# Performance work log

Measured on AMD Instinct MI355X. Metric: run time of the kernel, lower is better.

Reference implementation:

```python
import jax, jax.numpy as jnp
import numpy as np

B = 2_000_000
H = 4  # hidden size


def gru_cell(x, h, w_ih, w_hh, b_ih, b_hh):
    # torch GRUCell math. w_ih: [3H, in], w_hh: [3H, H]
    gi = x @ w_ih.T + b_ih  # [B, 3H]
    gh = h @ w_hh.T + b_hh  # [B, 3H]
    i_r, i_z, i_n = jnp.split(gi, 3, axis=1)
    h_r, h_z, h_n = jnp.split(gh, 3, axis=1)
    r = jax.nn.sigmoid(i_r + h_r)
    z = jax.nn.sigmoid(i_z + h_z)
    n = jnp.tanh(i_n + r * h_n)
    return (1.0 - z) * n + z * h


def setup_inputs() -> dict:
    key = jax.random.key(0)
    ks = jax.random.split(key, 16)
    s = 0.3  # small init scale
    inp = {
        "x": jax.random.normal(ks[0], (B, 18), dtype=jnp.float32),
        # r_up: GRUCell(2, 4)
        "w_ih_up": jax.random.normal(ks[1], (3 * H, 2), dtype=jnp.float32) * s,
        "w_hh_up": jax.random.normal(ks[2], (3 * H, H), dtype=jnp.float32) * s,
        "b_ih_up": jax.random.normal(ks[3], (3 * H,), dtype=jnp.float32) * s,
        "b_hh_up": jax.random.normal(ks[4], (3 * H,), dtype=jnp.float32) * s,
        # fc_obs_1: Linear(8, 4), fc_obs_2: Linear(4, 4)
        "w1": jax.random.normal(ks[5], (4, 8), dtype=jnp.float32) * s,
        "b1": jax.random.normal(ks[6], (4,), dtype=jnp.float32) * s,
        "w2": jax.random.normal(ks[7], (4, 4), dtype=jnp.float32) * s,
        "b2": jax.random.normal(ks[8], (4,), dtype=jnp.float32) * s,
        # r_down: GRUCell(4, 4)
        "w_ih_dn": jax.random.normal(ks[9], (3 * H, H), dtype=jnp.float32) * s,
        "w_hh_dn": jax.random.normal(ks[10], (3 * H, H), dtype=jnp.float32) * s,
        "b_ih_dn": jax.random.normal(ks[11], (3 * H,), dtype=jnp.float32) * s,
        "b_hh_dn": jax.random.normal(ks[12], (3 * H,), dtype=jnp.float32) * s,
        # fc_out: Linear(5, 1)
        "w_out": jax.random.normal(ks[13], (1, 5), dtype=jnp.float32) * s,
        "b_out": jax.random.normal(ks[14], (1,), dtype=jnp.float32) * s,
    }
    return inp


def reference(x, w_ih_up, w_hh_up, b_ih_up, b_hh_up, w1, b1, w2, b2,
              w_ih_dn, w_hh_dn, b_ih_dn, b_hh_dn, w_out, b_out):
    obs = x[:, :4]
    j = x[:, 4:11]    # [B, 7]
    jd = x[:, 11:18]  # [B, 7]
    b = x.shape[0]

    # upward recurrence over joints i = 6..0
    h = jnp.zeros((b, H), dtype=x.dtype)
    h_up = []
    for i in reversed(range(7)):
        xi = jnp.stack([j[:, i], jd[:, i]], axis=1)  # [B, 2]
        h = gru_cell(xi, h, w_ih_up, w_hh_up, b_ih_up, b_hh_up)
        h_up.append(h)

    # observation MLP fusion
    h = jnp.tanh(jnp.concatenate([obs, h], axis=1) @ w1.T + b1)
    h = jnp.tanh(h @ w2.T + b2)

    # downward recurrence i = 0..6 consuming h_up in append order
    acts = []
    for i in range(7):
        h = gru_cell(h_up[i], h, w_ih_dn, w_hh_dn, b_ih_dn, b_hh_dn)
        a = jnp.concatenate([h, j[:, i:i + 1]], axis=1) @ w_out.T + b_out  # [B, 1]
        acts.append(a)
    return jnp.concatenate(acts, axis=1)  # [B, 7]
```

## Files before the change

kernel.cpp:

```cpp
#include <hip/hip_runtime.h>


typedef float v2f __attribute__((ext_vector_type(2)));

__device__ __forceinline__ v2f mk2(float a, float b) { v2f r; r.x = a; r.y = b; return r; }
__device__ __forceinline__ v2f spl(float s) { return mk2(s, s); }
__device__ __forceinline__ v2f fma2(v2f a, v2f b, v2f c) { return __builtin_elementwise_fma(a, b, c); }

__device__ __forceinline__ float fexp2(float x) {
#if __has_builtin(__builtin_amdgcn_exp2f)
    return __builtin_amdgcn_exp2f(x);
#else
    return __expf(0.6931471805599453f * x);
#endif
}
__device__ __forceinline__ float frcp(float x) { return __builtin_amdgcn_rcpf(x); }

#define LOG2E 1.44269504088896f

__device__ __forceinline__ v2f sig2(v2f g) {
    v2f t = g * spl(-LOG2E);
    v2f e = mk2(fexp2(t.x), fexp2(t.y));
    v2f d = e + spl(1.0f);
    return mk2(frcp(d.x), frcp(d.y));
}
__device__ __forceinline__ v2f tanh2(v2f g) {
    v2f t = g * spl(-2.0f * LOG2E);
    v2f e = mk2(fexp2(t.x), fexp2(t.y));
    v2f d = e + spl(1.0f);
    v2f r = mk2(frcp(d.x), frcp(d.y));
    return fma2(r, spl(2.0f), spl(-1.0f));
}

__device__ __forceinline__ v2f dot4(const float* __restrict__ w, int k,
                                    v2f a, v2f b, v2f acc) {
    acc = fma2(spl(a.x), mk2(w[4 * k + 0], w[4 * k + 4]), acc);
    acc = fma2(spl(a.y), mk2(w[4 * k + 1], w[4 * k + 5]), acc);
    acc = fma2(spl(b.x), mk2(w[4 * k + 2], w[4 * k + 6]), acc);
    acc = fma2(spl(b.y), mk2(w[4 * k + 3], w[4 * k + 7]), acc);
    return acc;
}

__global__ void __launch_bounds__(256) trec_kernel(
    const float* __restrict__ x,
    const float* __restrict__ w_ih_up, const float* __restrict__ w_hh_up,
    const float* __restrict__ b_ih_up, const float* __restrict__ b_hh_up,
    const float* __restrict__ w1, const float* __restrict__ b1,
    const float* __restrict__ w2, const float* __restrict__ b2,
    const float* __restrict__ w_ih_dn, const float* __restrict__ w_hh_dn,
    const float* __restrict__ b_ih_dn, const float* __restrict__ b_hh_dn,
    const float* __restrict__ w_out, const float* __restrict__ b_out,
    float* __restrict__ out, int n)
{
    int row = blockIdx.x * blockDim.x + threadIdx.x;
    if (row >= n) return;

    float xv[18];
    {
        const float2* xp = reinterpret_cast<const float2*>(x + (size_t)row * 18u);
        #pragma unroll
        for (int k = 0; k < 9; ++k) {
            float2 v = xp[k];
            xv[2 * k] = v.x;
            xv[2 * k + 1] = v.y;
        }
    }

    v2f bsum_up[4], bsum_dn[4];
    #pragma unroll
    for (int p = 0; p < 4; ++p) {
        bsum_up[p] = mk2(b_ih_up[2 * p], b_ih_up[2 * p + 1]) + mk2(b_hh_up[2 * p], b_hh_up[2 * p + 1]);
        bsum_dn[p] = mk2(b_ih_dn[2 * p], b_ih_dn[2 * p + 1]) + mk2(b_hh_dn[2 * p], b_hh_dn[2 * p + 1]);
    }
    const v2f bihnA_up = mk2(b_ih_up[8], b_ih_up[9]),  bihnB_up = mk2(b_ih_up[10], b_ih_up[11]);
    const v2f bhhnA_up = mk2(b_hh_up[8], b_hh_up[9]),  bhhnB_up = mk2(b_hh_up[10], b_hh_up[11]);
    const v2f bihnA_dn = mk2(b_ih_dn[8], b_ih_dn[9]),  bihnB_dn = mk2(b_ih_dn[10], b_ih_dn[11]);
    const v2f bhhnA_dn = mk2(b_hh_dn[8], b_hh_dn[9]),  bhhnB_dn = mk2(b_hh_dn[10], b_hh_dn[11]);

    v2f hA = spl(0.f), hB = spl(0.f);
    v2f hupA[7], hupB[7];

    #pragma unroll
    for (int s = 0; s < 7; ++s) {
        const int i = 6 - s;
        const v2f X0 = spl(xv[4 + i]);
        const v2f X1 = spl(xv[11 + i]);

        v2f rz[4];
        #pragma unroll
        for (int p = 0; p < 4; ++p) {
            const int k = 2 * p;
            v2f acc = bsum_up[p];
            acc = fma2(X0, mk2(w_ih_up[2 * k], w_ih_up[2 * k + 2]), acc);
            acc = fma2(X1, mk2(w_ih_up[2 * k + 1], w_ih_up[2 * k + 3]), acc);
            acc = dot4(w_hh_up, k, hA, hB, acc);
            rz[p] = acc;
        }
        v2f rA = sig2(rz[0]), rB = sig2(rz[1]);
        v2f zA = sig2(rz[2]), zB = sig2(rz[3]);

        v2f giA = bihnA_up, giB = bihnB_up;
        giA = fma2(X0, mk2(w_ih_up[16], w_ih_up[18]), giA);
        giA = fma2(X1, mk2(w_ih_up[17], w_ih_up[19]), giA);
        giB = fma2(X0, mk2(w_ih_up[20], w_ih_up[22]), giB);
        giB = fma2(X1, mk2(w_ih_up[21], w_ih_up[23]), giB);
        v2f ghA = dot4(w_hh_up, 8,  hA, hB, bhhnA_up);
        v2f ghB = dot4(w_hh_up, 10, hA, hB, bhhnB_up);
        v2f nA = tanh2(fma2(rA, ghA, giA));
        v2f nB = tanh2(fma2(rB, ghB, giB));

        hA = fma2(zA, hA - nA, nA);
        hB = fma2(zB, hB - nB, nB);
        hupA[s] = hA; hupB[s] = hB;
    }

    {
        float in8[8] = { xv[0], xv[1], xv[2], xv[3], hA.x, hA.y, hB.x, hB.y };
        v2f t1A, t1B;
        {
            v2f a0 = mk2(b1[0], b1[1]), a1 = mk2(b1[2], b1[3]);
            #pragma unroll
            for (int d = 0; d < 8; ++d) {
                a0 = fma2(spl(in8[d]), mk2(w1[d], w1[8 + d]), a0);
                a1 = fma2(spl(in8[d]), mk2(w1[16 + d], w1[24 + d]), a1);
            }
            t1A = tanh2(a0); t1B = tanh2(a1);
        }
        v2f a0 = dot4(w2, 0, t1A, t1B, mk2(b2[0], b2[1]));
        v2f a1 = dot4(w2, 2, t1A, t1B, mk2(b2[2], b2[3]));
        hA = tanh2(a0); hB = tanh2(a1);
    }

    const float wo0 = w_out[0], wo1 = w_out[1], wo2 = w_out[2], wo3 = w_out[3], wo4 = w_out[4];
    const float bo = b_out[0];
    float acts[7];
    #pragma unroll
    for (int i = 0; i < 7; ++i) {
        const v2f xiA = hupA[i], xiB = hupB[i];

        v2f rz[4];
        #pragma unroll
        for (int p = 0; p < 4; ++p) {
            const int k = 2 * p;
            v2f acc = bsum_dn[p];
            acc = dot4(w_ih_dn, k, xiA, xiB, acc);
            acc = dot4(w_hh_dn, k, hA, hB, acc);
            rz[p] = acc;
        }
        v2f rA = sig2(rz[0]), rB = sig2(rz[1]);
        v2f zA = sig2(rz[2]), zB = sig2(rz[3]);

        v2f giA = dot4(w_ih_dn, 8,  xiA, xiB, bihnA_dn);
        v2f giB = dot4(w_ih_dn, 10, xiA, xiB, bihnB_dn);
        v2f ghA = dot4(w_hh_dn, 8,  hA, hB, bhhnA_dn);
        v2f ghB = dot4(w_hh_dn, 10, hA, hB, bhhnB_dn);
        v2f nA = tanh2(fma2(rA, ghA, giA));
        v2f nB = tanh2(fma2(rB, ghB, giB));

        hA = fma2(zA, hA - nA, nA);
        hB = fma2(zB, hB - nB, nB);

        v2f t = fma2(hA, mk2(wo0, wo1), mk2(bo, 0.f));
        t = fma2(hB, mk2(wo2, wo3), t);
        acts[i] = fmaf(xv[4 + i], wo4, t.x + t.y);
    }

    float* op = out + (size_t)row * 7u;
    #pragma unroll
    for (int i = 0; i < 7; ++i) op[i] = acts[i];
}

extern "C" void kernel_launch(void* const* d_in, const int* in_sizes, int n_in,
                              void* d_out, int out_size, void* d_ws, size_t ws_size,
                              hipStream_t stream)
{
    const float* x       = (const float*)d_in[0];
    const float* w_ih_up = (const float*)d_in[1];
    const float* w_hh_up = (const float*)d_in[2];
    const float* b_ih_up = (const float*)d_in[3];
    const float* b_hh_up = (const float*)d_in[4];
    const float* w1      = (const float*)d_in[5];
    const float* b1      = (const float*)d_in[6];
    const float* w2      = (const float*)d_in[7];
    const float* b2      = (const float*)d_in[8];
    const float* w_ih_dn = (const float*)d_in[9];
    const float* w_hh_dn = (const float*)d_in[10];
    const float* b_ih_dn = (const float*)d_in[11];
    const float* b_hh_dn = (const float*)d_in[12];
    const float* w_out   = (const float*)d_in[13];
    const float* b_out   = (const float*)d_in[14];
    float* out = (float*)d_out;

    const int n = in_sizes[0] / 18;
    const int block = 256;
    const int grid = (n + block - 1) / block;

    trec_kernel<<<grid, block, 0, stream>>>(
        x, w_ih_up, w_hh_up, b_ih_up, b_hh_up,
        w1, b1, w2, b2,
        w_ih_dn, w_hh_dn, b_ih_dn, b_hh_dn,
        w_out, b_out, out, n);
}
```

Measured before the change: 112.7 us.

## Use packed fp16 dot2 instructions for GRU matvecs with repacked weights

Adds a tiny repack kernel that sums biases and converts all weights to packed fp16 pairs in the workspace. The main kernel then computes every gate and MLP dot product with v_dot2_f32_f16 on fp16-packed hidden states, inputs and weights, accumulating in fp32. This roughly halves the ALU instruction count and the scalar weight loads, at the cost of fp16 rounding of weights and activations, which may push results past the tolerance, plus one extra launch per call.

```diff
diff --git a/kernel.cpp b/kernel.cpp
--- a/kernel.cpp
+++ b/kernel.cpp
@@ -2,6 +2,7 @@
 
 
 typedef float v2f __attribute__((ext_vector_type(2)));
+typedef __fp16 h2 __attribute__((ext_vector_type(2)));
 
 __device__ __forceinline__ v2f mk2(float a, float b) { v2f r; r.x = a; r.y = b; return r; }
 __device__ __forceinline__ v2f spl(float s) { return mk2(s, s); }
@@ -32,17 +33,19 @@
     return fma2(r, spl(2.0f), spl(-1.0f));
 }
 
-__device__ __forceinline__ v2f dot4(const float* __restrict__ w, int k,
-                                    v2f a, v2f b, v2f acc) {
-    acc = fma2(spl(a.x), mk2(w[4 * k + 0], w[4 * k + 4]), acc);
-    acc = fma2(spl(a.y), mk2(w[4 * k + 1], w[4 * k + 5]), acc);
-    acc = fma2(spl(b.x), mk2(w[4 * k + 2], w[4 * k + 6]), acc);
-    acc = fma2(spl(b.y), mk2(w[4 * k + 3], w[4 * k + 7]), acc);
-    return acc;
-}
-
-__global__ void __launch_bounds__(256) trec_kernel(
-    const float* __restrict__ x,
+__device__ __forceinline__ float fdot2(h2 a, h2 b, float c) {
+#if __has_builtin(__builtin_amdgcn_fdot2)
+    return __builtin_amdgcn_fdot2(a, b, c, false);
+#else
+    return fmaf((float)a.x, (float)b.x, fmaf((float)a.y, (float)b.y, c));
+#endif
+}
+__device__ __forceinline__ h2 pkh(float a, float b) {
+    return __builtin_amdgcn_cvt_pkrtz(a, b);
+}
+
+
+__global__ void repack_kernel(
     const float* __restrict__ w_ih_up, const float* __restrict__ w_hh_up,
     const float* __restrict__ b_ih_up, const float* __restrict__ b_hh_up,
     const float* __restrict__ w1, const float* __restrict__ b1,
@@ -50,10 +53,51 @@
     const float* __restrict__ w_ih_dn, const float* __restrict__ w_hh_dn,
     const float* __restrict__ b_ih_dn, const float* __restrict__ b_hh_dn,
     const float* __restrict__ w_out, const float* __restrict__ b_out,
+    float* __restrict__ ws)
+{
+    const int t = threadIdx.x;
+    if (t < 42) {
+        float v;
+        if      (t < 8)  v = b_ih_up[t] + b_hh_up[t];
+        else if (t < 16) v = b_ih_dn[t - 8] + b_hh_dn[t - 8];
+        else if (t < 20) v = b_ih_up[8 + t - 16];
+        else if (t < 24) v = b_hh_up[8 + t - 20];
+        else if (t < 28) v = b_ih_dn[8 + t - 24];
+        else if (t < 32) v = b_hh_dn[8 + t - 28];
+        else if (t < 36) v = b1[t - 32];
+        else if (t < 40) v = b2[t - 36];
+        else if (t == 40) v = w_out[4];
+        else              v = b_out[0];
+        ws[t] = v;
+    } else if (t < 152) {
+        const int u = t - 42;
+        float a, b;
+        if (u < 12)       { a = w_ih_up[2*u];                          b = w_ih_up[2*u + 1]; }
+        else if (u < 36)  { int v = u - 12, k = v >> 1, e = v & 1;     a = w_hh_up[4*k + 2*e]; b = w_hh_up[4*k + 2*e + 1]; }
+        else if (u < 60)  { int v = u - 36, k = v >> 1, e = v & 1;     a = w_ih_dn[4*k + 2*e]; b = w_ih_dn[4*k + 2*e + 1]; }
+        else if (u < 84)  { int v = u - 60, k = v >> 1, e = v & 1;     a = w_hh_dn[4*k + 2*e]; b = w_hh_dn[4*k + 2*e + 1]; }
+        else if (u < 100) { int v = u - 84, k = v >> 2, c = v & 3;     a = w1[8*k + 2*c];      b = w1[8*k + 2*c + 1]; }
+        else if (u < 108) { int v = u - 100, k = v >> 1, c = v & 1;    a = w2[4*k + 2*c];      b = w2[4*k + 2*c + 1]; }
+        else              { int c = u - 108;                           a = w_out[2*c];         b = w_out[2*c + 1]; }
+        reinterpret_cast<h2*>(ws)[t] = pkh(a, b);
+    }
+}
+
+__global__ void __launch_bounds__(256) trec_kernel(
+    const float* __restrict__ x, const float* __restrict__ sb,
     float* __restrict__ out, int n)
 {
-    int row = blockIdx.x * blockDim.x + threadIdx.x;
+    const int row = blockIdx.x * blockDim.x + threadIdx.x;
     if (row >= n) return;
+
+    const h2* __restrict__ wh = reinterpret_cast<const h2*>(sb + 42);
+    #define WIU(k)    wh[(k)]
+    #define WHU(k,e)  wh[12 + 2*(k) + (e)]
+    #define WID(k,e)  wh[36 + 2*(k) + (e)]
+    #define WHD(k,e)  wh[60 + 2*(k) + (e)]
+    #define W1H(k,c)  wh[84 + 4*(k) + (c)]
+    #define W2H(k,c)  wh[100 + 2*(k) + (c)]
+    #define WOH(c)    wh[108 + (c)]
 
     float xv[18];
     {
@@ -65,109 +109,99 @@
             xv[2 * k + 1] = v.y;
         }
     }
-
-    v2f bsum_up[4], bsum_dn[4];
-    #pragma unroll
-    for (int p = 0; p < 4; ++p) {
-        bsum_up[p] = mk2(b_ih_up[2 * p], b_ih_up[2 * p + 1]) + mk2(b_hh_up[2 * p], b_hh_up[2 * p + 1]);
-        bsum_dn[p] = mk2(b_ih_dn[2 * p], b_ih_dn[2 * p + 1]) + mk2(b_hh_dn[2 * p], b_hh_dn[2 * p + 1]);
-    }
-    const v2f bihnA_up = mk2(b_ih_up[8], b_ih_up[9]),  bihnB_up = mk2(b_ih_up[10], b_ih_up[11]);
-    const v2f bhhnA_up = mk2(b_hh_up[8], b_hh_up[9]),  bhhnB_up = mk2(b_hh_up[10], b_hh_up[11]);
-    const v2f bihnA_dn = mk2(b_ih_dn[8], b_ih_dn[9]),  bihnB_dn = mk2(b_ih_dn[10], b_ih_dn[11]);
-    const v2f bhhnA_dn = mk2(b_hh_dn[8], b_hh_dn[9]),  bhhnB_dn = mk2(b_hh_dn[10], b_hh_dn[11]);
+    h2 xjh[7];
+    #pragma unroll
+    for (int i = 0; i < 7; ++i) xjh[i] = pkh(xv[4 + i], xv[11 + i]);
 
     v2f hA = spl(0.f), hB = spl(0.f);
-    v2f hupA[7], hupB[7];
+    h2 h01 = pkh(0.f, 0.f), h23 = pkh(0.f, 0.f);
+    h2 hup01[7], hup23[7];
 
     #pragma unroll
     for (int s = 0; s < 7; ++s) {
         const int i = 6 - s;
-        const v2f X0 = spl(xv[4 + i]);
-        const v2f X1 = spl(xv[11 + i]);
-
-        v2f rz[4];
-        #pragma unroll
-        for (int p = 0; p < 4; ++p) {
-            const int k = 2 * p;
-            v2f acc = bsum_up[p];
-            acc = fma2(X0, mk2(w_ih_up[2 * k], w_ih_up[2 * k + 2]), acc);
-            acc = fma2(X1, mk2(w_ih_up[2 * k + 1], w_ih_up[2 * k + 3]), acc);
-            acc = dot4(w_hh_up, k, hA, hB, acc);
-            rz[p] = acc;
+        const h2 xh = xjh[i];
+
+        float g[8];
+        #pragma unroll
+        for (int k = 0; k < 8; ++k)
+            g[k] = fdot2(h23, WHU(k, 1), fdot2(h01, WHU(k, 0), fdot2(xh, WIU(k), sb[k])));
+        v2f rA = sig2(mk2(g[0], g[1])), rB = sig2(mk2(g[2], g[3]));
+        v2f zA = sig2(mk2(g[4], g[5])), zB = sig2(mk2(g[6], g[7]));
+
+        float gi[4], gh[4];
+        #pragma unroll
+        for (int k = 0; k < 4; ++k) {
+            gi[k] = fdot2(xh, WIU(8 + k), sb[16 + k]);
+            gh[k] = fdot2(h23, WHU(8 + k, 1), fdot2(h01, WHU(8 + k, 0), sb[20 + k]));
         }
-        v2f rA = sig2(rz[0]), rB = sig2(rz[1]);
-        v2f zA = sig2(rz[2]), zB = sig2(rz[3]);
-
-        v2f giA = bihnA_up, giB = bihnB_up;
-        giA = fma2(X0, mk2(w_ih_up[16], w_ih_up[18]), giA);
-        giA = fma2(X1, mk2(w_ih_up[17], w_ih_up[19]), giA);
-        giB = fma2(X0, mk2(w_ih_up[20], w_ih_up[22]), giB);
-        giB = fma2(X1, mk2(w_ih_up[21], w_ih_up[23]), giB);
-        v2f ghA = dot4(w_hh_up, 8,  hA, hB, bhhnA_up);
-        v2f ghB = dot4(w_hh_up, 10, hA, hB, bhhnB_up);
-        v2f nA = tanh2(fma2(rA, ghA, giA));
-        v2f nB = tanh2(fma2(rB, ghB, giB));
+        v2f nA = tanh2(fma2(rA, mk2(gh[0], gh[1]), mk2(gi[0], gi[1])));
+        v2f nB = tanh2(fma2(rB, mk2(gh[2], gh[3]), mk2(gi[2], gi[3])));
 
         hA = fma2(zA, hA - nA, nA);
         hB = fma2(zB, hB - nB, nB);
-        hupA[s] = hA; hupB[s] = hB;
+        h01 = pkh(hA.x, hA.y); h23 = pkh(hB.x, hB.y);
+        hup01[s] = h01; hup23[s] = h23;
     }
 
     {
-        float in8[8] = { xv[0], xv[1], xv[2], xv[3], hA.x, hA.y, hB.x, hB.y };
-        v2f t1A, t1B;
-        {
-            v2f a0 = mk2(b1[0], b1[1]), a1 = mk2(b1[2], b1[3]);
-            #pragma unroll
-            for (int d = 0; d < 8; ++d) {
-                a0 = fma2(spl(in8[d]), mk2(w1[d], w1[8 + d]), a0);
-                a1 = fma2(spl(in8[d]), mk2(w1[16 + d], w1[24 + d]), a1);
-            }
-            t1A = tanh2(a0); t1B = tanh2(a1);
+        h2 o01 = pkh(xv[0], xv[1]), o23 = pkh(xv[2], xv[3]);
+        float a[4];
+        #pragma unroll
+        for (int k = 0; k < 4; ++k)
+            a[k] = fdot2(h23, W1H(k, 3), fdot2(h01, W1H(k, 2),
+                    fdot2(o23, W1H(k, 1), fdot2(o01, W1H(k, 0), sb[32 + k]))));
+        v2f t1A = tanh2(mk2(a[0], a[1])), t1B = tanh2(mk2(a[2], a[3]));
+        h2 t01 = pkh(t1A.x, t1A.y), t23 = pkh(t1B.x, t1B.y);
+        float c[4];
+        #pragma unroll
+        for (int k = 0; k < 4; ++k)
+            c[k] = fdot2(t23, W2H(k, 1), fdot2(t01, W2H(k, 0), sb[36 + k]));
+        hA = tanh2(mk2(c[0], c[1])); hB = tanh2(mk2(c[2], c[3]));
+        h01 = pkh(hA.x, hA.y); h23 = pkh(hB.x, hB.y);
+    }
+
+    const float wo4 = sb[40], bo = sb[41];
+    float acts[7];
+    #pragma unroll
+    for (int i = 0; i < 7; ++i) {
+        const h2 xi01 = hup01[i], xi23 = hup23[i];
+
+        float g[8];
+        #pragma unroll
+        for (int k = 0; k < 8; ++k)
+            g[k] = fdot2(h23, WHD(k, 1), fdot2(h01, WHD(k, 0),
+                    fdot2(xi23, WID(k, 1), fdot2(xi01, WID(k, 0), sb[8 + k]))));
+        v2f rA = sig2(mk2(g[0], g[1])), rB = sig2(mk2(g[2], g[3]));
+        v2f zA = sig2(mk2(g[4], g[5])), zB = sig2(mk2(g[6], g[7]));
+
+        float gi[4], gh[4];
+        #pragma unroll
+        for (int k = 0; k < 4; ++k) {
+            gi[k] = fdot2(xi23, WID(8 + k, 1), fdot2(xi01, WID(8 + k, 0), sb[24 + k]));
+            gh[k] = fdot2(h23, WHD(8 + k, 1), fdot2(h01, WHD(8 + k, 0), sb[28 + k]));
         }
-        v2f a0 = dot4(w2, 0, t1A, t1B, mk2(b2[0], b2[1]));
-        v2f a1 = dot4(w2, 2, t1A, t1B, mk2(b2[2], b2[3]));
-        hA = tanh2(a0); hB = tanh2(a1);
-    }
-
-    const float wo0 = w_out[0], wo1 = w_out[1], wo2 = w_out[2], wo3 = w_out[3], wo4 = w_out[4];
-    const float bo = b_out[0];
-    float acts[7];
-    #pragma unroll
-    for (int i = 0; i < 7; ++i) {
-        const v2f xiA = hupA[i], xiB = hupB[i];
-
-        v2f rz[4];
-        #pragma unroll
-        for (int p = 0; p < 4; ++p) {
-            const int k = 2 * p;
-            v2f acc = bsum_dn[p];
-            acc = dot4(w_ih_dn, k, xiA, xiB, acc);
-            acc = dot4(w_hh_dn, k, hA, hB, acc);
-            rz[p] = acc;
-        }
-        v2f rA = sig2(rz[0]), rB = sig2(rz[1]);
-        v2f zA = sig2(rz[2]), zB = sig2(rz[3]);
-
-        v2f giA = dot4(w_ih_dn, 8,  xiA, xiB, bihnA_dn);
-        v2f giB = dot4(w_ih_dn, 10, xiA, xiB, bihnB_dn);
-        v2f ghA = dot4(w_hh_dn, 8,  hA, hB, bhhnA_dn);
-        v2f ghB = dot4(w_hh_dn, 10, hA, hB, bhhnB_dn);
-        v2f nA = tanh2(fma2(rA, ghA, giA));
-        v2f nB = tanh2(fma2(rB, ghB, giB));
+        v2f nA = tanh2(fma2(rA, mk2(gh[0], gh[1]), mk2(gi[0], gi[1])));
+        v2f nB = tanh2(fma2(rB, mk2(gh[2], gh[3]), mk2(gi[2], gi[3])));
 
         hA = fma2(zA, hA - nA, nA);
         hB = fma2(zB, hB - nB, nB);
-
-        v2f t = fma2(hA, mk2(wo0, wo1), mk2(bo, 0.f));
-        t = fma2(hB, mk2(wo2, wo3), t);
-        acts[i] = fmaf(xv[4 + i], wo4, t.x + t.y);
+        h01 = pkh(hA.x, hA.y); h23 = pkh(hB.x, hB.y);
+
+        acts[i] = fmaf(xv[4 + i], wo4, fdot2(h23, WOH(1), fdot2(h01, WOH(0), bo)));
     }
 
     float* op = out + (size_t)row * 7u;
     #pragma unroll
     for (int i = 0; i < 7; ++i) op[i] = acts[i];
+
+    #undef WIU
+    #undef WHU
+    #undef WID
+    #undef WHD
+    #undef W1H
+    #undef W2H
+    #undef WOH
 }
 
 extern "C" void kernel_launch(void* const* d_in, const int* in_sizes, int n_in,
@@ -195,9 +229,12 @@
     const int block = 256;
     const int grid = (n + block - 1) / block;
 
-    trec_kernel<<<grid, block, 0, stream>>>(
-        x, w_ih_up, w_hh_up, b_ih_up, b_hh_up,
+    repack_kernel<<<1, 192, 0, stream>>>(
+        w_ih_up, w_hh_up, b_ih_up, b_hh_up,
         w1, b1, w2, b2,
         w_ih_dn, w_hh_dn, b_ih_dn, b_hh_dn,
-        w_out, b_out, out, n);
-}
+        w_out, b_out, (float*)d_ws);
+
+    trec_kernel<<<grid, block, 0, stream>>>(
+        x, (const float*)d_ws, out, n);
+}
```

Measured after the change: 117.0 us. +3.8%, slower.
